# Kernel optimization log

Hardware: AMD Instinct MI355X
Metric: run time of the kernel (lower is better)

## Reference

```python
import jax, jax.numpy as jnp
import numpy as np

NPOINT = 512
RADIUS = 0.1
NSAMPLE = 32
MLP_DIMS = [67, 64, 64, 128]  # 3 (rel xyz) + 64 feature channels -> ... -> 128


def setup_inputs() -> dict:
    key = jax.random.key(0)
    ks = jax.random.split(key, 8)
    N, C = 65536, 64
    xyz = jax.random.uniform(ks[0], (N, 3), dtype=jnp.float32)
    features = jax.random.normal(ks[1], (C, N), dtype=jnp.float32)
    inp = {"xyz": xyz, "features": features, "num_points": 8192}
    for i in range(3):
        cin, cout = MLP_DIMS[i], MLP_DIMS[i + 1]
        inp[f"W{i}"] = jax.random.normal(ks[2 + i], (cout, cin), dtype=jnp.float32) / np.sqrt(cin).astype(np.float32)
        inp[f"b{i}"] = jnp.zeros((cout,), jnp.float32)
    return inp


def _fps(pts, npoint):
    """Furthest point sampling for one example. pts: [n,3] -> [npoint] int32."""
    n = pts.shape[0]
    d0 = jnp.full((n,), 1e10, pts.dtype)

    def body(carry, _):
        dist, last = carry
        d = jnp.sum((pts - pts[last]) ** 2, axis=-1)
        dist = jnp.minimum(dist, d)
        nxt = jnp.argmax(dist).astype(jnp.int32)
        return (dist, nxt), nxt

    (_, _), rest = jax.lax.scan(body, (d0, jnp.int32(0)), None, length=npoint - 1)
    return jnp.concatenate([jnp.zeros((1,), jnp.int32), rest])


def _ball_query(centers, pts, radius, nsample):
    """centers: [m,3], pts: [n,3] -> [m,nsample] int32 (first nsample in-ball ids,
    padded with the first in-ball id, matching pointnet2 ball_query semantics)."""
    m = centers.shape[0]
    n = pts.shape[0]
    d2 = jnp.sum((centers[:, None, :] - pts[None, :, :]) ** 2, axis=-1)  # [m, n]
    mask = d2 < radius * radius
    pos = jnp.cumsum(mask.astype(jnp.int32), axis=-1)  # rank of each in-ball point
    first = jnp.argmax(mask, axis=-1).astype(jnp.int32)  # first in-ball idx (0 if none)
    default = jnp.broadcast_to(first[:, None], (m, nsample))
    # extra dump column at slot==nsample for out-of-ball / overflow entries
    init = jnp.concatenate([default, jnp.zeros((m, 1), jnp.int32)], axis=1)
    slot = jnp.where(mask & (pos <= nsample), pos - 1, nsample)  # [m, n]
    rows = jnp.broadcast_to(jnp.arange(m)[:, None], (m, n))
    cols = jnp.broadcast_to(jnp.arange(n, dtype=jnp.int32)[None, :], (m, n))
    idx = init.at[rows, slot].set(cols)
    return idx[:, :nsample]


def reference(xyz, features, num_points, W0, b0, W1, b1, W2, b2):
    N = xyz.shape[0]
    B = N // num_points
    C = features.shape[0]
    xyz_b = xyz.reshape(B, num_points, 3)                      # [B, n, 3]
    feat_b = features.reshape(C, B, num_points).transpose(1, 0, 2)  # [B, C, n]

    # FPS per example
    new_idx = jax.vmap(lambda p: _fps(p, NPOINT))(xyz_b)        # [B, npoint]
    new_xyz = jnp.take_along_axis(xyz_b, new_idx[..., None], axis=1)  # [B, npoint, 3]

    # ball query + grouping (QueryAndGroup, use_xyz=True)
    sample_ids = jax.vmap(lambda c, p: _ball_query(c, p, RADIUS, NSAMPLE))(new_xyz, xyz_b)  # [B, npoint, nsample]
    grouped_xyz = jax.vmap(lambda p, i: p[i])(xyz_b, sample_ids)      # [B, npoint, nsample, 3]
    grouped_xyz = grouped_xyz - new_xyz[:, :, None, :]                # relative coords
    grouped_feat = jax.vmap(lambda f, i: f[:, i])(feat_b, sample_ids)  # [B, C, npoint, nsample]
    g = jnp.concatenate([grouped_xyz.transpose(0, 3, 1, 2), grouped_feat], axis=1)  # [B, 3+C, npoint, nsample]

    # shared 1x1 conv MLP + ReLU, then max over the nsample dim
    h = g
    for W, b in ((W0, b0), (W1, b1), (W2, b2)):
        h = jax.nn.relu(jnp.einsum('oc,bcps->bops', W, h) + b[None, :, None, None])
    new_features = h.max(axis=-1)  # [B, 128, npoint]

    return new_xyz, new_idx, new_features, sample_ids
```

## Files before the change

kernel.cpp:

```cpp
#include <hip/hip_runtime.h>
#include <cstdint>
#include <cstddef>

#define NPOINT 512
#define NSAMPLE 32
#define NPB 8192

__device__ __forceinline__ unsigned short f2bf(float f) {
  unsigned int u = __float_as_uint(f);
  unsigned int r = u + 0x7FFFu + ((u >> 16) & 1u);
  return (unsigned short)(r >> 16);
}

#define FPS_UPD(J)                                                             \
  do {                                                                         \
    float dx_ = __fsub_rn(px##J, qx);                                          \
    float dy_ = __fsub_rn(py##J, qy);                                          \
    float dz_ = __fsub_rn(pz##J, qz);                                          \
    float s_ = __fadd_rn(__fadd_rn(__fmul_rn(dx_, dx_), __fmul_rn(dy_, dy_)),  \
                         __fmul_rn(dz_, dz_));                                 \
    d##J = fminf(d##J, s_);                                                    \
  } while (0)

#define FPS_CHK(J)                                                             \
  if (d##J == wmax) { bi = J; wx = px##J; wy = py##J; wz = pz##J; }

__global__ __launch_bounds__(512, 2) void k_fps(const float* __restrict__ xyz,
                                                float* __restrict__ out_xyz,
                                                float* __restrict__ out_idx) {
  const int b = blockIdx.x;
  const int t = threadIdx.x;
  const float* xb = xyz + (size_t)b * NPB * 3;

  const float4* gp = reinterpret_cast<const float4*>(xb + (size_t)t * 48);
  float4 v0 = gp[0], v1 = gp[1], v2 = gp[2], v3 = gp[3];
  float4 v4 = gp[4], v5 = gp[5], v6 = gp[6], v7 = gp[7];
  float4 v8 = gp[8], v9 = gp[9], v10 = gp[10], v11 = gp[11];
  float px0 = v0.x,  py0 = v0.y,  pz0 = v0.z;
  float px1 = v0.w,  py1 = v1.x,  pz1 = v1.y;
  float px2 = v1.z,  py2 = v1.w,  pz2 = v2.x;
  float px3 = v2.y,  py3 = v2.z,  pz3 = v2.w;
  float px4 = v3.x,  py4 = v3.y,  pz4 = v3.z;
  float px5 = v3.w,  py5 = v4.x,  pz5 = v4.y;
  float px6 = v4.z,  py6 = v4.w,  pz6 = v5.x;
  float px7 = v5.y,  py7 = v5.z,  pz7 = v5.w;
  float px8 = v6.x,  py8 = v6.y,  pz8 = v6.z;
  float px9 = v6.w,  py9 = v7.x,  pz9 = v7.y;
  float px10 = v7.z, py10 = v7.w, pz10 = v8.x;
  float px11 = v8.y, py11 = v8.z, pz11 = v8.w;
  float px12 = v9.x, py12 = v9.y, pz12 = v9.z;
  float px13 = v9.w, py13 = v10.x, pz13 = v10.y;
  float px14 = v10.z, py14 = v10.w, pz14 = v11.x;
  float px15 = v11.y, py15 = v11.z, pz15 = v11.w;

  asm volatile("" : "+v"(px0), "+v"(py0), "+v"(pz0), "+v"(px1), "+v"(py1),
                    "+v"(pz1), "+v"(px2), "+v"(py2));
  asm volatile("" : "+v"(pz2), "+v"(px3), "+v"(py3), "+v"(pz3), "+v"(px4),
                    "+v"(py4), "+v"(pz4), "+v"(px5));
  asm volatile("" : "+v"(py5), "+v"(pz5), "+v"(px6), "+v"(py6), "+v"(pz6),
                    "+v"(px7), "+v"(py7), "+v"(pz7));
  asm volatile("" : "+v"(px8), "+v"(py8), "+v"(pz8), "+v"(px9), "+v"(py9),
                    "+v"(pz9), "+v"(px10), "+v"(py10));
  asm volatile("" : "+v"(pz10), "+v"(px11), "+v"(py11), "+v"(pz11),
                    "+v"(px12), "+v"(py12), "+v"(pz12), "+v"(px13));
  asm volatile("" : "+v"(py13), "+v"(pz13), "+v"(px14), "+v"(py14),
                    "+v"(pz14), "+v"(px15), "+v"(py15), "+v"(pz15));

  float d0 = 1e10f, d1 = 1e10f, d2 = 1e10f, d3 = 1e10f;
  float d4 = 1e10f, d5 = 1e10f, d6 = 1e10f, d7 = 1e10f;
  float d8 = 1e10f, d9 = 1e10f, d10 = 1e10f, d11 = 1e10f;
  float d12 = 1e10f, d13 = 1e10f, d14 = 1e10f, d15 = 1e10f;

  __shared__ __align__(16) float sD[2][8];
  __shared__ int sI[2][8];
  __shared__ float sX[2][8], sY[2][8], sZ[2][8];

  const int wid = t >> 6;
  const int lane = t & 63;

  float qx = xb[0], qy = xb[1], qz = xb[2];
  if (t == 0) {
    out_idx[b * NPOINT + 0] = 0.0f;
    size_t o = (size_t)(b * NPOINT) * 3;
    out_xyz[o + 0] = qx; out_xyz[o + 1] = qy; out_xyz[o + 2] = qz;
  }

  for (int it = 1; it < NPOINT; ++it) {
    FPS_UPD(0);  FPS_UPD(1);  FPS_UPD(2);  FPS_UPD(3);
    FPS_UPD(4);  FPS_UPD(5);  FPS_UPD(6);  FPS_UPD(7);
    FPS_UPD(8);  FPS_UPD(9);  FPS_UPD(10); FPS_UPD(11);
    FPS_UPD(12); FPS_UPD(13); FPS_UPD(14); FPS_UPD(15);
    float m01 = fmaxf(d0, d1),   m23 = fmaxf(d2, d3);
    float m45 = fmaxf(d4, d5),   m67 = fmaxf(d6, d7);
    float m89 = fmaxf(d8, d9),   mab = fmaxf(d10, d11);
    float mcd = fmaxf(d12, d13), mef = fmaxf(d14, d15);
    float q0 = fmaxf(fmaxf(m01, m23), fmaxf(m45, m67));
    float q1 = fmaxf(fmaxf(m89, mab), fmaxf(mcd, mef));
    float best = fmaxf(q0, q1);
    float wmax = best;
#pragma unroll
    for (int off = 32; off >= 1; off >>= 1) wmax = fmaxf(wmax, __shfl_xor(wmax, off));
    const unsigned long long m = __ballot(best == wmax);
    const int p = it & 1;
    if (lane == (int)(__ffsll((unsigned long long)m) - 1)) {
      int bi = 15; float wx = px15, wy = py15, wz = pz15;
      FPS_CHK(14) FPS_CHK(13) FPS_CHK(12) FPS_CHK(11)
      FPS_CHK(10) FPS_CHK(9)  FPS_CHK(8)  FPS_CHK(7)
      FPS_CHK(6)  FPS_CHK(5)  FPS_CHK(4)  FPS_CHK(3)
      FPS_CHK(2)  FPS_CHK(1)  FPS_CHK(0)
      sD[p][wid] = wmax;
      sI[p][wid] = t * 16 + bi;
      sX[p][wid] = wx; sY[p][wid] = wy; sZ[p][wid] = wz;
    }
    __syncthreads();
    float bd = sD[p][0];
    int bw = 0;
#pragma unroll
    for (int w = 1; w < 8; ++w) {
      float d_ = sD[p][w];
      if (d_ > bd) { bd = d_; bw = w; }
    }
    const int gbi = sI[p][bw];
    qx = sX[p][bw]; qy = sY[p][bw]; qz = sZ[p][bw];
    if (t == 0) {
      out_idx[b * NPOINT + it] = (float)gbi;
      size_t o = (size_t)(b * NPOINT + it) * 3;
      out_xyz[o + 0] = qx; out_xyz[o + 1] = qy; out_xyz[o + 2] = qz;
    }
  }
}

__global__ __launch_bounds__(256) void k_transpose(const float* __restrict__ in,
                                                   unsigned short* __restrict__ out,
                                                   int Ntot) {
  __shared__ __align__(16) unsigned short tile[64][65];
  const int t = threadIdx.x;
  const int n0 = blockIdx.x * 64;
#pragma unroll
  for (int i = 0; i < 16; ++i) {
    int c = i * 4 + (t >> 6);
    int n = t & 63;
    tile[c][n] = f2bf(in[(size_t)c * Ntot + n0 + n]);
  }
  __syncthreads();
#pragma unroll
  for (int i = 0; i < 16; ++i) {
    int n = i * 4 + (t >> 6);
    int c = t & 63;
    out[(size_t)(n0 + n) * 64 + c] = tile[c][n];
  }
}

__global__ __launch_bounds__(512) void k_ball(const float* __restrict__ xyz,
                                              const float* __restrict__ fps_idx_f,
                                              float* __restrict__ sids_f) {
  __shared__ int slots[8 * NSAMPLE];
  const int b = blockIdx.x >> 6;
  const int cbase = (blockIdx.x & 63) * 8;
  const int t = threadIdx.x;
  const float* xb = xyz + (size_t)b * NPB * 3;

  const int w = t >> 6, lane = t & 63;
  const int c_local = cbase + w;
  const int ci = (int)fps_idx_f[b * NPOINT + c_local];
  const float cx = xb[ci * 3 + 0];
  const float cy = xb[ci * 3 + 1];
  const float cz = xb[ci * 3 + 2];
  const float R2 = 0.01f;
  const unsigned long long below = (1ull << lane) - 1ull;

  int cnt = 0;
#pragma unroll 4
  for (int r = 0; r < 64; ++r) {
    const int p0 = r * 128 + lane;
    const int p1 = p0 + 64;
    float ax = xb[p0 * 3 + 0], ay = xb[p0 * 3 + 1], az = xb[p0 * 3 + 2];
    float bx = xb[p1 * 3 + 0], by = xb[p1 * 3 + 1], bz = xb[p1 * 3 + 2];
    float dxa = __fsub_rn(ax, cx), dya = __fsub_rn(ay, cy), dza = __fsub_rn(az, cz);
    float dxb = __fsub_rn(bx, cx), dyb = __fsub_rn(by, cy), dzb = __fsub_rn(bz, cz);
    float d2a = __fadd_rn(__fadd_rn(__fmul_rn(dxa, dxa), __fmul_rn(dya, dya)), __fmul_rn(dza, dza));
    float d2b = __fadd_rn(__fadd_rn(__fmul_rn(dxb, dxb), __fmul_rn(dyb, dyb)), __fmul_rn(dzb, dzb));
    const bool i0 = d2a < R2;
    const bool i1 = d2b < R2;
    const unsigned long long m0 = __ballot(i0);
    if (i0) {
      int pos = cnt + (int)__popcll(m0 & below);
      if (pos < NSAMPLE) slots[w * NSAMPLE + pos] = p0;
    }
    cnt += (int)__popcll(m0);
    const unsigned long long m1 = __ballot(i1);
    if (i1) {
      int pos = cnt + (int)__popcll(m1 & below);
      if (pos < NSAMPLE) slots[w * NSAMPLE + pos] = p1;
    }
    cnt += (int)__popcll(m1);
  }
  if (lane < NSAMPLE) {
    const int first = (cnt > 0) ? slots[w * NSAMPLE] : 0;
    const int v = (lane < cnt) ? slots[w * NSAMPLE + lane] : first;
    sids_f[((size_t)(b * NPOINT + c_local)) * NSAMPLE + lane] = (float)v;
  }
}

__global__ __launch_bounds__(256) void k_mlp(const float* __restrict__ xyz,
                                             const float* __restrict__ feat,
                                             const unsigned short* __restrict__ feat_t,
                                             const float* __restrict__ fps_idx_f,
                                             const float* __restrict__ sids_f,
                                             const float* __restrict__ w0g,
                                             const float* __restrict__ b0g,
                                             const float* __restrict__ w1g,
                                             const float* __restrict__ b1g,
                                             const float* __restrict__ w2g,
                                             const float* __restrict__ b2g,
                                             float* __restrict__ out_feat,
                                             int Ntot, int useT) {
  __shared__ __align__(16) float W0s[64 * 68];
  __shared__ __align__(16) unsigned short W1s[64 * 64];
  __shared__ __align__(16) float W2s[128 * 64];
  __shared__ float b0s[64], b1s[64], b2s[128];
  const int t = threadIdx.x;
  for (int i = t; i < 64 * 68; i += 256) {
    int r = i / 68, c = i - r * 68;
    W0s[i] = (c < 67) ? w0g[r * 67 + c] : 0.0f;
  }
  for (int i = t; i < 64 * 64; i += 256) W1s[i] = f2bf(w1g[i]);
  for (int i = t; i < 128 * 64; i += 256) W2s[i] = w2g[i];
  if (t < 64) b0s[t] = b0g[t];
  if (t < 64) b1s[t] = b1g[t];
  if (t < 128) b2s[t] = b2g[t];
  __syncthreads();

  const int b = blockIdx.x >> 6;
  const int c_local = (blockIdx.x & 63) * 8 + (t >> 5);
  const int s = t & 31;
  const int ci = (int)fps_idx_f[b * NPOINT + c_local];
  const float cx = xyz[((size_t)b * NPB + ci) * 3 + 0];
  const float cy = xyz[((size_t)b * NPB + ci) * 3 + 1];
  const float cz = xyz[((size_t)b * NPB + ci) * 3 + 2];
  const int id = (int)sids_f[((size_t)(b * NPOINT + c_local)) * NSAMPLE + s];

  float g[68];
  {
    const size_t pb = ((size_t)b * NPB + id) * 3;
    g[0] = __fsub_rn(xyz[pb + 0], cx);
    g[1] = __fsub_rn(xyz[pb + 1], cy);
    g[2] = __fsub_rn(xyz[pb + 2], cz);
    if (useT) {
      const uint4* fp = reinterpret_cast<const uint4*>(feat_t + ((size_t)b * NPB + id) * 64);
#pragma unroll
      for (int v = 0; v < 8; ++v) {
        uint4 r = fp[v];
        unsigned int vs[4] = {r.x, r.y, r.z, r.w};
#pragma unroll
        for (int q = 0; q < 4; ++q) {
          g[3 + v * 8 + q * 2 + 0] = __uint_as_float(vs[q] << 16);
          g[3 + v * 8 + q * 2 + 1] = __uint_as_float(vs[q] & 0xFFFF0000u);
        }
      }
    } else {
      const float* col = feat + (size_t)(b * NPB + id);
#pragma unroll 8
      for (int c = 0; c < 64; ++c) g[3 + c] = col[(size_t)c * Ntot];
    }
    g[67] = 0.0f;
  }

  float h1[64];
#pragma unroll
  for (int o = 0; o < 64; ++o) {
    float acc = b0s[o];
    const float4* wp = reinterpret_cast<const float4*>(&W0s[o * 68]);
#pragma unroll
    for (int c4 = 0; c4 < 17; ++c4) {
      float4 wv = wp[c4];
      acc += wv.x * g[c4 * 4 + 0];
      acc += wv.y * g[c4 * 4 + 1];
      acc += wv.z * g[c4 * 4 + 2];
      acc += wv.w * g[c4 * 4 + 3];
    }
    h1[o] = fmaxf(acc, 0.0f);
  }
  float h2[64];
#pragma unroll
  for (int o = 0; o < 64; ++o) {
    float acc = b1s[o];
    const uint2* wp = reinterpret_cast<const uint2*>(&W1s[o * 64]);
#pragma unroll
    for (int c4 = 0; c4 < 16; ++c4) {
      uint2 u = wp[c4];
      acc += __uint_as_float(u.x << 16) * h1[c4 * 4 + 0];
      acc += __uint_as_float(u.x & 0xFFFF0000u) * h1[c4 * 4 + 1];
      acc += __uint_as_float(u.y << 16) * h1[c4 * 4 + 2];
      acc += __uint_as_float(u.y & 0xFFFF0000u) * h1[c4 * 4 + 3];
    }
    h2[o] = fmaxf(acc, 0.0f);
  }
#pragma unroll 1
  for (int o = 0; o < 128; ++o) {
    float acc = b2s[o];
    const float4* wp = reinterpret_cast<const float4*>(&W2s[o * 64]);
#pragma unroll
    for (int c4 = 0; c4 < 16; ++c4) {
      float4 wv = wp[c4];
      acc += wv.x * h2[c4 * 4 + 0];
      acc += wv.y * h2[c4 * 4 + 1];
      acc += wv.z * h2[c4 * 4 + 2];
      acc += wv.w * h2[c4 * 4 + 3];
    }
    float v = fmaxf(acc, 0.0f);
#pragma unroll
    for (int off = 16; off >= 1; off >>= 1) v = fmaxf(v, __shfl_xor(v, off));
    if (s == 0) out_feat[((size_t)b * 128 + o) * NPOINT + c_local] = v;
  }
}

extern "C" void kernel_launch(void* const* d_in, const int* in_sizes, int n_in,
                              void* d_out, int out_size, void* d_ws, size_t ws_size,
                              hipStream_t stream) {
  (void)n_in; (void)out_size;
  const float* xyz = (const float*)d_in[0];
  const float* feat = (const float*)d_in[1];
  const float* w0 = (const float*)d_in[3];
  const float* b0 = (const float*)d_in[4];
  const float* w1 = (const float*)d_in[5];
  const float* b1 = (const float*)d_in[6];
  const float* w2 = (const float*)d_in[7];
  const float* b2 = (const float*)d_in[8];

  const int Ntot = in_sizes[0] / 3;
  const int B = Ntot / NPB;

  float* out = (float*)d_out;
  float* o_xyz = out;
  float* o_idx = o_xyz + (size_t)B * NPOINT * 3;
  float* o_feat = o_idx + (size_t)B * NPOINT;
  float* o_sids = o_feat + (size_t)B * 128 * NPOINT;

  const size_t ft_bytes = (size_t)Ntot * 64 * 2;
  const int useT = (ws_size >= ft_bytes) ? 1 : 0;
  unsigned short* ft_ws = (unsigned short*)d_ws;

  if (useT) {
    k_transpose<<<dim3(Ntot / 64), dim3(256), 0, stream>>>(feat, ft_ws, Ntot);
  }
  k_fps<<<dim3(B), dim3(512), 0, stream>>>(xyz, o_xyz, o_idx);
  k_ball<<<dim3(B * 64), dim3(512), 0, stream>>>(xyz, o_idx, o_sids);
  k_mlp<<<dim3(B * 64), dim3(256), 0, stream>>>(xyz, feat, ft_ws, o_idx, o_sids,
                                                w0, b0, w1, b1, w2, b2, o_feat,
                                                Ntot, useT);
}
```

Baseline: 919.6 us.

## Split FPS across 1024 threads with 8 points each and packed winner slots

The furthest-point-sampling kernel now runs 1024 threads per example, each holding 8 points instead of 16. This halves the serial per-thread distance update and max-reduction work on every one of the 511 dependent iterations. Each wave's winner is packed into one float4 (xyz plus index as float), and the cross-wave argmax reads four float4s from shared memory. The cost is 16 waves per block to synchronise each iteration and a longer cross-wave scan. Only 8 blocks launch, so the GPU is mostly idle either way.

New measurement: 936.5 us. About the same (+1.8%).

```diff
diff --git a/kernel.cpp b/kernel.cpp
--- a/kernel.cpp
+++ b/kernel.cpp
@@ -25,33 +25,27 @@
 #define FPS_CHK(J)                                                             \
   if (d##J == wmax) { bi = J; wx = px##J; wy = py##J; wz = pz##J; }
 
-__global__ __launch_bounds__(512, 2) void k_fps(const float* __restrict__ xyz,
-                                                float* __restrict__ out_xyz,
-                                                float* __restrict__ out_idx) {
+#define FPS_SCAN(W, EXPR)                                                      \
+  do { float e_ = (EXPR); if (e_ > bd) { bd = e_; bw = W; } } while (0)
+
+__global__ __launch_bounds__(1024, 4) void k_fps(const float* __restrict__ xyz,
+                                                 float* __restrict__ out_xyz,
+                                                 float* __restrict__ out_idx) {
   const int b = blockIdx.x;
   const int t = threadIdx.x;
   const float* xb = xyz + (size_t)b * NPB * 3;
 
-  const float4* gp = reinterpret_cast<const float4*>(xb + (size_t)t * 48);
-  float4 v0 = gp[0], v1 = gp[1], v2 = gp[2], v3 = gp[3];
-  float4 v4 = gp[4], v5 = gp[5], v6 = gp[6], v7 = gp[7];
-  float4 v8 = gp[8], v9 = gp[9], v10 = gp[10], v11 = gp[11];
-  float px0 = v0.x,  py0 = v0.y,  pz0 = v0.z;
-  float px1 = v0.w,  py1 = v1.x,  pz1 = v1.y;
-  float px2 = v1.z,  py2 = v1.w,  pz2 = v2.x;
-  float px3 = v2.y,  py3 = v2.z,  pz3 = v2.w;
-  float px4 = v3.x,  py4 = v3.y,  pz4 = v3.z;
-  float px5 = v3.w,  py5 = v4.x,  pz5 = v4.y;
-  float px6 = v4.z,  py6 = v4.w,  pz6 = v5.x;
-  float px7 = v5.y,  py7 = v5.z,  pz7 = v5.w;
-  float px8 = v6.x,  py8 = v6.y,  pz8 = v6.z;
-  float px9 = v6.w,  py9 = v7.x,  pz9 = v7.y;
-  float px10 = v7.z, py10 = v7.w, pz10 = v8.x;
-  float px11 = v8.y, py11 = v8.z, pz11 = v8.w;
-  float px12 = v9.x, py12 = v9.y, pz12 = v9.z;
-  float px13 = v9.w, py13 = v10.x, pz13 = v10.y;
-  float px14 = v10.z, py14 = v10.w, pz14 = v11.x;
-  float px15 = v11.y, py15 = v11.z, pz15 = v11.w;
+  const float4* gp = reinterpret_cast<const float4*>(xb + (size_t)t * 24);
+  float4 v0 = gp[0], v1 = gp[1], v2 = gp[2];
+  float4 v3 = gp[3], v4 = gp[4], v5 = gp[5];
+  float px0 = v0.x, py0 = v0.y, pz0 = v0.z;
+  float px1 = v0.w, py1 = v1.x, pz1 = v1.y;
+  float px2 = v1.z, py2 = v1.w, pz2 = v2.x;
+  float px3 = v2.y, py3 = v2.z, pz3 = v2.w;
+  float px4 = v3.x, py4 = v3.y, pz4 = v3.z;
+  float px5 = v3.w, py5 = v4.x, pz5 = v4.y;
+  float px6 = v4.z, py6 = v4.w, pz6 = v5.x;
+  float px7 = v5.y, py7 = v5.z, pz7 = v5.w;
 
   asm volatile("" : "+v"(px0), "+v"(py0), "+v"(pz0), "+v"(px1), "+v"(py1),
                     "+v"(pz1), "+v"(px2), "+v"(py2));
@@ -59,21 +53,12 @@
                     "+v"(py4), "+v"(pz4), "+v"(px5));
   asm volatile("" : "+v"(py5), "+v"(pz5), "+v"(px6), "+v"(py6), "+v"(pz6),
                     "+v"(px7), "+v"(py7), "+v"(pz7));
-  asm volatile("" : "+v"(px8), "+v"(py8), "+v"(pz8), "+v"(px9), "+v"(py9),
-                    "+v"(pz9), "+v"(px10), "+v"(py10));
-  asm volatile("" : "+v"(pz10), "+v"(px11), "+v"(py11), "+v"(pz11),
-                    "+v"(px12), "+v"(py12), "+v"(pz12), "+v"(px13));
-  asm volatile("" : "+v"(py13), "+v"(pz13), "+v"(px14), "+v"(py14),
-                    "+v"(pz14), "+v"(px15), "+v"(py15), "+v"(pz15));
 
   float d0 = 1e10f, d1 = 1e10f, d2 = 1e10f, d3 = 1e10f;
   float d4 = 1e10f, d5 = 1e10f, d6 = 1e10f, d7 = 1e10f;
-  float d8 = 1e10f, d9 = 1e10f, d10 = 1e10f, d11 = 1e10f;
-  float d12 = 1e10f, d13 = 1e10f, d14 = 1e10f, d15 = 1e10f;
-
-  __shared__ __align__(16) float sD[2][8];
-  __shared__ int sI[2][8];
-  __shared__ float sX[2][8], sY[2][8], sZ[2][8];
+
+  __shared__ __align__(16) float sD[2][16];
+  __shared__ __align__(16) float4 sWin[2][16];
 
   const int wid = t >> 6;
   const int lane = t & 63;
@@ -86,44 +71,36 @@
   }
 
   for (int it = 1; it < NPOINT; ++it) {
-    FPS_UPD(0);  FPS_UPD(1);  FPS_UPD(2);  FPS_UPD(3);
-    FPS_UPD(4);  FPS_UPD(5);  FPS_UPD(6);  FPS_UPD(7);
-    FPS_UPD(8);  FPS_UPD(9);  FPS_UPD(10); FPS_UPD(11);
-    FPS_UPD(12); FPS_UPD(13); FPS_UPD(14); FPS_UPD(15);
-    float m01 = fmaxf(d0, d1),   m23 = fmaxf(d2, d3);
-    float m45 = fmaxf(d4, d5),   m67 = fmaxf(d6, d7);
-    float m89 = fmaxf(d8, d9),   mab = fmaxf(d10, d11);
-    float mcd = fmaxf(d12, d13), mef = fmaxf(d14, d15);
-    float q0 = fmaxf(fmaxf(m01, m23), fmaxf(m45, m67));
-    float q1 = fmaxf(fmaxf(m89, mab), fmaxf(mcd, mef));
-    float best = fmaxf(q0, q1);
+    FPS_UPD(0); FPS_UPD(1); FPS_UPD(2); FPS_UPD(3);
+    FPS_UPD(4); FPS_UPD(5); FPS_UPD(6); FPS_UPD(7);
+    float m01 = fmaxf(d0, d1), m23 = fmaxf(d2, d3);
+    float m45 = fmaxf(d4, d5), m67 = fmaxf(d6, d7);
+    float best = fmaxf(fmaxf(m01, m23), fmaxf(m45, m67));
     float wmax = best;
 #pragma unroll
     for (int off = 32; off >= 1; off >>= 1) wmax = fmaxf(wmax, __shfl_xor(wmax, off));
     const unsigned long long m = __ballot(best == wmax);
     const int p = it & 1;
     if (lane == (int)(__ffsll((unsigned long long)m) - 1)) {
-      int bi = 15; float wx = px15, wy = py15, wz = pz15;
-      FPS_CHK(14) FPS_CHK(13) FPS_CHK(12) FPS_CHK(11)
-      FPS_CHK(10) FPS_CHK(9)  FPS_CHK(8)  FPS_CHK(7)
-      FPS_CHK(6)  FPS_CHK(5)  FPS_CHK(4)  FPS_CHK(3)
-      FPS_CHK(2)  FPS_CHK(1)  FPS_CHK(0)
+      int bi = 7; float wx = px7, wy = py7, wz = pz7;
+      FPS_CHK(6) FPS_CHK(5) FPS_CHK(4) FPS_CHK(3)
+      FPS_CHK(2) FPS_CHK(1) FPS_CHK(0)
       sD[p][wid] = wmax;
-      sI[p][wid] = t * 16 + bi;
-      sX[p][wid] = wx; sY[p][wid] = wy; sZ[p][wid] = wz;
+      sWin[p][wid] = make_float4(wx, wy, wz, (float)(t * 8 + bi));
     }
     __syncthreads();
-    float bd = sD[p][0];
+    const float4* sd4 = reinterpret_cast<const float4*>(&sD[p][0]);
+    float4 a0 = sd4[0], a1 = sd4[1], a2 = sd4[2], a3 = sd4[3];
+    float bd = a0.x;
     int bw = 0;
-#pragma unroll
-    for (int w = 1; w < 8; ++w) {
-      float d_ = sD[p][w];
-      if (d_ > bd) { bd = d_; bw = w; }
-    }
-    const int gbi = sI[p][bw];
-    qx = sX[p][bw]; qy = sY[p][bw]; qz = sZ[p][bw];
+    FPS_SCAN(1, a0.y);  FPS_SCAN(2, a0.z);  FPS_SCAN(3, a0.w);
+    FPS_SCAN(4, a1.x);  FPS_SCAN(5, a1.y);  FPS_SCAN(6, a1.z);  FPS_SCAN(7, a1.w);
+    FPS_SCAN(8, a2.x);  FPS_SCAN(9, a2.y);  FPS_SCAN(10, a2.z); FPS_SCAN(11, a2.w);
+    FPS_SCAN(12, a3.x); FPS_SCAN(13, a3.y); FPS_SCAN(14, a3.z); FPS_SCAN(15, a3.w);
+    float4 win = sWin[p][bw];
+    qx = win.x; qy = win.y; qz = win.z;
     if (t == 0) {
-      out_idx[b * NPOINT + it] = (float)gbi;
+      out_idx[b * NPOINT + it] = win.w;
       size_t o = (size_t)(b * NPOINT + it) * 3;
       out_xyz[o + 0] = qx; out_xyz[o + 1] = qy; out_xyz[o + 2] = qz;
     }
@@ -344,7 +321,7 @@
   if (useT) {
     k_transpose<<<dim3(Ntot / 64), dim3(256), 0, stream>>>(feat, ft_ws, Ntot);
   }
-  k_fps<<<dim3(B), dim3(512), 0, stream>>>(xyz, o_xyz, o_idx);
+  k_fps<<<dim3(B), dim3(1024), 0, stream>>>(xyz, o_xyz, o_idx);
   k_ball<<<dim3(B * 64), dim3(512), 0, stream>>>(xyz, o_idx, o_sids);
   k_mlp<<<dim3(B * 64), dim3(256), 0, stream>>>(xyz, feat, ft_ws, o_idx, o_sids,
                                                 w0, b0, w1, b1, w2, b2, o_feat,
```
